# Kernel tuning notes

Hardware: AMD Instinct MI355X
Metric: run time of the kernel (lower is better)

Reference implementation:

```python
import jax, jax.numpy as jnp
import numpy as np

MU_P = 0.15
MASK_ID = 103
VOCAB = 30522


def setup_inputs() -> dict:
    key = jax.random.key(0)
    k1, k2 = jax.random.split(key)
    B, C, S = 1024, 4, 2048
    # first half = per-token sampling weights, second half = shared_tokens (unused by the math)
    my_attention_mask = jax.random.uniform(k1, (B, C, 2 * S), dtype=jnp.float32)
    attention_mask = jnp.ones((B, C, S), dtype=jnp.int32)  # tokenizer attention mask
    input_ids = jax.random.randint(k2, (B, C, S), 0, VOCAB, dtype=jnp.int32)
    return {"my_attention_mask": my_attention_mask,
            "attention_mask": attention_mask,
            "input_ids": input_ids}


def reference(my_attention_mask, attention_mask, input_ids):
    """Weighted sampling WITHOUT replacement per (batch, choice) row via Gumbel-top-k.

    Original loops over (k, j), draws num_to_mask = floor(sum(tok_mask) * N(mu_p, sigma))
    indices from the nonzero weights in my_attention_mask[..., :S] (prob ~ weight),
    masks those token positions in input_ids and emits the indicator mask.
    Gumbel-top-k: keys = log(w) + Gumbel noise; the top-num_to_mask keys are a
    weighted sample without replacement from w. Zero-weight positions get -inf keys.
    """
    B, C, S = input_ids.shape
    w = my_attention_mask[..., :S]  # [B, C, S] sampling weights

    key = jax.random.key(42)
    kg, kn = jax.random.split(key)
    sigma = min(0.05, MU_P / 4.0)
    frac = MU_P + sigma * jax.random.normal(kn, (B, C), dtype=jnp.float32)
    num_to_mask = jnp.floor(
        attention_mask.sum(axis=-1).astype(jnp.float32) * frac
    ).astype(jnp.int32)  # [B, C]

    log_w = jnp.where(w > 0, jnp.log(jnp.maximum(w, 1e-30)), -jnp.inf)
    keys = log_w + jax.random.gumbel(kg, w.shape, dtype=jnp.float32)  # [B, C, S]

    # rank[i] = position of i in descending key order (double argsort)
    order = jnp.argsort(-keys, axis=-1)
    rank = jnp.argsort(order, axis=-1)
    new_attention_mask = (rank < num_to_mask[..., None]).astype(jnp.int32)  # [B, C, S]

    new_input_ids = jnp.where(new_attention_mask == 1, MASK_ID, input_ids)
    discriminator_labels = -new_attention_mask
    return new_input_ids, new_attention_mask, discriminator_labels
```

## Files before the change

kernel.cpp:

```cpp
#include <hip/hip_runtime.h>
#include <stdint.h>
#include <math.h>

#define SLEN 2048
#define EPT 32
#define NTHREADS 256
#define ROWS_PER_BLOCK 4
#define NCHUNK 8
#define TOKENS_PER_OUT 8388608

__host__ __device__ __forceinline__ void tf2x32(uint32_t k0, uint32_t k1,
                                                uint32_t x0, uint32_t x1,
                                                uint32_t &o0, uint32_t &o1) {
  uint32_t ks2 = 0x1BD11BDAu ^ k0 ^ k1;
  x0 += k0; x1 += k1;
#define TFR(r) { x0 += x1; x1 = (x1 << (r)) | (x1 >> (32 - (r))); x1 ^= x0; }
  TFR(13) TFR(15) TFR(26) TFR(6)
  x0 += k1;  x1 += ks2 + 1u;
  TFR(17) TFR(29) TFR(16) TFR(24)
  x0 += ks2; x1 += k0 + 2u;
  TFR(13) TFR(15) TFR(26) TFR(6)
  x0 += k0;  x1 += k1 + 3u;
  TFR(17) TFR(29) TFR(16) TFR(24)
  x0 += k1;  x1 += ks2 + 4u;
  TFR(13) TFR(15) TFR(26) TFR(6)
  x0 += ks2; x1 += k0 + 5u;
#undef TFR
  o0 = x0; o1 = x1;
}

__device__ __forceinline__ void tf4_bits(uint32_t k0, uint32_t k1,
                                         uint32_t cbase, uint32_t bits[4]) {
  const uint32_t ks2 = 0x1BD11BDAu ^ k0 ^ k1;
  uint32_t x0[4], x1[4];
#pragma unroll
  for (int i = 0; i < 4; ++i) { x0[i] = k0; x1[i] = (cbase + (uint32_t)i) + k1; }
#define TFR4(r)                                                         \
  _Pragma("unroll")                                                     \
  for (int i = 0; i < 4; ++i) {                                         \
    x0[i] += x1[i];                                                     \
    x1[i] = (x1[i] << (r)) | (x1[i] >> (32 - (r)));                     \
    x1[i] ^= x0[i];                                                     \
  }                                                                     \
  __builtin_amdgcn_sched_barrier(0);
#define INJ4(a, b)                                                      \
  _Pragma("unroll")                                                     \
  for (int i = 0; i < 4; ++i) { x0[i] += (a); x1[i] += (b); }
  TFR4(13) TFR4(15) TFR4(26) TFR4(6)
  INJ4(k1, ks2 + 1u)
  TFR4(17) TFR4(29) TFR4(16) TFR4(24)
  INJ4(ks2, k0 + 2u)
  TFR4(13) TFR4(15) TFR4(26) TFR4(6)
  INJ4(k0, k1 + 3u)
  TFR4(17) TFR4(29) TFR4(16) TFR4(24)
  INJ4(k1, ks2 + 4u)
  TFR4(13) TFR4(15) TFR4(26) TFR4(6)
  INJ4(ks2, k0 + 5u)
#undef TFR4
#undef INJ4
#pragma unroll
  for (int i = 0; i < 4; ++i) bits[i] = x0[i] ^ x1[i];
}

__device__ __forceinline__ float u01_from_bits(uint32_t bits) {
  return __uint_as_float((bits >> 9) | 0x3F800000u) - 1.0f;
}

#define SBAR() __builtin_amdgcn_sched_barrier(0)

template<int CTRL, int RMASK>
__device__ __forceinline__ uint32_t dpp_mov0(uint32_t x) {
  return (uint32_t)__builtin_amdgcn_update_dpp(0, (int)x, CTRL, RMASK, 0xF, false);
}
__device__ __forceinline__ uint32_t wave_incl_scan(uint32_t x) {
  x += dpp_mov0<0x111, 0xF>(x);
  x += dpp_mov0<0x112, 0xF>(x);
  x += dpp_mov0<0x114, 0xF>(x);
  x += dpp_mov0<0x118, 0xF>(x);
  x += dpp_mov0<0x142, 0xA>(x);
  x += dpp_mov0<0x143, 0xC>(x);
  return x;
}

__device__ __forceinline__ void log8_cr(const float x[8], float out[8]) {
#pragma clang fp contract(off)
  double m[8]; int e[8];
#pragma unroll
  for (int i = 0; i < 8; ++i) {
    uint32_t xb   = __float_as_uint(x[i]);
    uint32_t mant = xb & 0x7FFFFFu;
    int      ee   = (int)(xb >> 23) - 127;
    bool     big  = mant > 0x3504F3u;
    e[i] = ee + (big ? 1 : 0);
    uint32_t hi = (big ? 0x3FE00000u : 0x3FF00000u) | (mant >> 3);
    uint32_t lo = mant << 29;
    m[i] = __longlong_as_double(((long long)hi << 32) | (long long)lo);
  }
  SBAR();
  double mp1[8];
#pragma unroll
  for (int i = 0; i < 8; ++i) mp1[i] = m[i] + 1.0;
  SBAR();
  double y[8];
#pragma unroll
  for (int i = 0; i < 8; ++i) y[i] = __builtin_amdgcn_rcp(mp1[i]);
  SBAR();
#pragma unroll
  for (int i = 0; i < 8; ++i) y[i] = fma(fma(-mp1[i], y[i], 1.0), y[i], y[i]);
  SBAR();
  double r[8];
#pragma unroll
  for (int i = 0; i < 8; ++i) r[i] = (m[i] - 1.0) * y[i];
  SBAR();
  double t[8];
#pragma unroll
  for (int i = 0; i < 8; ++i) t[i] = r[i] * r[i];
  SBAR();
  double p[8];
#pragma unroll
  for (int i = 0; i < 8; ++i) p[i] = fma(0.07692307692307693, t[i], 0.09090909090909091);
  SBAR();
#pragma unroll
  for (int i = 0; i < 8; ++i) p[i] = fma(p[i], t[i], 0.1111111111111111);
  SBAR();
#pragma unroll
  for (int i = 0; i < 8; ++i) p[i] = fma(p[i], t[i], 0.14285714285714285);
  SBAR();
#pragma unroll
  for (int i = 0; i < 8; ++i) p[i] = fma(p[i], t[i], 0.2);
  SBAR();
#pragma unroll
  for (int i = 0; i < 8; ++i) p[i] = fma(p[i], t[i], 0.3333333333333333);
  SBAR();
#pragma unroll
  for (int i = 0; i < 8; ++i) p[i] = fma(p[i], t[i], 1.0);
  SBAR();
#pragma unroll
  for (int i = 0; i < 8; ++i) r[i] = r[i] + r[i];
  SBAR();
#pragma unroll
  for (int i = 0; i < 8; ++i) p[i] = r[i] * p[i];
  SBAR();
#pragma unroll
  for (int i = 0; i < 8; ++i)
    out[i] = (float)fma((double)e[i], 0.6931471805599453, p[i]);
}

__device__ __forceinline__ float log_cr(float x) {
#pragma clang fp contract(off)
  uint32_t xb   = __float_as_uint(x);
  uint32_t mant = xb & 0x7FFFFFu;
  int      e    = (int)(xb >> 23) - 127;
  bool     big  = mant > 0x3504F3u;
  e += big ? 1 : 0;
  uint32_t hi = (big ? 0x3FE00000u : 0x3FF00000u) | (mant >> 3);
  double m = __longlong_as_double(((long long)hi << 32) | (long long)(mant << 29));
  double mp1 = m + 1.0;
  double y = __builtin_amdgcn_rcp(mp1);
  y = fma(fma(-mp1, y, 1.0), y, y);
  double r = (m - 1.0) * y;
  double t = r * r;
  double p = fma(0.07692307692307693, t, 0.09090909090909091);
  p = fma(p, t, 0.1111111111111111);
  p = fma(p, t, 0.14285714285714285);
  p = fma(p, t, 0.2);
  p = fma(p, t, 0.3333333333333333);
  p = fma(p, t, 1.0);
  return (float)fma((double)e, 0.6931471805599453, (r + r) * p);
}

__device__ float erfinv_xla(float x) {
#pragma clang fp contract(off)
  float x2  = x * x;
  float nx2 = -x2;
  float l1p;
  if (fabsf(nx2) < 1e-4f) {
    l1p = (-0.5f * nx2 + 1.0f) * nx2;
  } else {
    l1p = log_cr(1.0f + nx2);
  }
  float w = -l1p;
  float p;
  if (w < 5.0f) {
    float ww = w - 2.5f;
    p = 2.81022636e-08f;
    p = p * ww + 3.43273939e-07f;
    p = p * ww + -3.5233877e-06f;
    p = p * ww + -4.39150654e-06f;
    p = p * ww + 0.00021858087f;
    p = p * ww + -0.00125372503f;
    p = p * ww + -0.00417768164f;
    p = p * ww + 0.246640727f;
    p = p * ww + 1.50140941f;
  } else {
    float ww = sqrtf(w) - 3.0f;
    p = -0.000200214257f;
    p = p * ww + 0.000100950558f;
    p = p * ww + 0.00134934322f;
    p = p * ww + -0.00367342844f;
    p = p * ww + 0.00573950773f;
    p = p * ww + -0.0076224613f;
    p = p * ww + 0.00943887047f;
    p = p * ww + 1.00167406f;
    p = p * ww + 2.83297682f;
  }
  return p * x;
}

__global__ __launch_bounds__(NTHREADS, 4)
void gumbel_topk_mask(const float* __restrict__ wfull,
                      const int*   __restrict__ attn,
                      const int*   __restrict__ ids,
                      int* __restrict__ out,
                      uint32_t kg0, uint32_t kg1, uint32_t kn0, uint32_t kn1) {
#pragma clang fp contract(off)
  const int t    = threadIdx.x;
  const int lane = t & 63;
  const int wid  = t >> 6;
  const int row  = blockIdx.x * ROWS_PER_BLOCK + wid;

  __shared__ __align__(16) uint32_t hist[ROWS_PER_BLOCK][4][256];

  const size_t rbase = (size_t)row * SLEN;
  const size_t wbase = (size_t)row * (2 * SLEN);

#pragma unroll
  for (int p4 = 0; p4 < 4; ++p4)
    ((uint4*)hist[wid][p4])[lane] = make_uint4(0u, 0u, 0u, 0u);

  const int4*   av4 = (const int4*)(attn + rbase);
  const float4* wv4 = (const float4*)(wfull + wbase);
  const int4*   iv4 = (const int4*)(ids + rbase);

  int psum = 0;
#pragma unroll
  for (int j = 0; j < NCHUNK; ++j) {
    int4 a = av4[64 * j + lane];
    psum += a.x + a.y + a.z + a.w;
  }
  float4 wC[NCHUNK];
#pragma unroll
  for (int j = 0; j < NCHUNK; ++j) wC[j] = wv4[64 * j + lane];

  uint32_t no0, no1;
  tf2x32(kn0, kn1, 0u, (uint32_t)row, no0, no1);
  float f0  = u01_from_bits(no0 ^ no1);
  float lo  = __uint_as_float(0xBF7FFFFFu);
  float u2  = fmaxf(lo, f0 * 2.0f + lo);
  float z   = erfinv_xla(u2);
  float nrm = 1.4142135623730951f * z;
  float frac = 0.15f + 0.0375f * nrm;

  uint32_t ps = wave_incl_scan((uint32_t)psum);
  int asum = (int)__builtin_amdgcn_readlane((int)ps, 63);
  int kk = (int)floorf((float)asum * frac);

  uint32_t mloc[EPT];
#pragma unroll
  for (int c = 0; c < 4; ++c) {
    float4 wa = wC[2 * c], wb = wC[2 * c + 1];
    uint32_t bits[8];
    tf4_bits(kg0, kg1, (uint32_t)(rbase + 256 * (2 * c)     + 4 * lane), bits + 0);
    tf4_bits(kg0, kg1, (uint32_t)(rbase + 256 * (2 * c + 1) + 4 * lane), bits + 4);
    SBAR();
    float wl8[8] = {wa.x, wa.y, wa.z, wa.w, wb.x, wb.y, wb.z, wb.w};
    float uu[8];
#pragma unroll
    for (int e = 0; e < 8; ++e) {
      float f = u01_from_bits(bits[e]);
      uu[e] = fmaxf(1.17549435e-38f, f * 1.0f + 1.17549435e-38f);
    }
    SBAR();
    float l1[8];
    log8_cr(uu, l1);
    float wm[8];
#pragma unroll
    for (int e = 0; e < 8; ++e) wm[e] = fmaxf(wl8[e], 1e-30f);
    float lw[8];
    log8_cr(wm, lw);
    float nl1[8];
#pragma unroll
    for (int e = 0; e < 8; ++e) nl1[e] = -l1[e];
    float l2[8];
    log8_cr(nl1, l2);
    SBAR();
#pragma unroll
    for (int e = 0; e < 8; ++e) {
      float key = (wl8[e] > 0.0f) ? (lw[e] + (-l2[e])) : -__builtin_inff();
      uint32_t kb = __float_as_uint(key);
      mloc[8 * c + e] = (kb & 0x80000000u) ? ~kb : (kb | 0x80000000u);
    }
  }

  int4 idsv[NCHUNK];
#pragma unroll
  for (int j = 0; j < NCHUNK; ++j) idsv[j] = iv4[64 * j + lane];

  uint32_t T, r;
  if (kk <= 0)          { T = 0xFFFFFFFFu; r = 0u; }
  else if (kk >= SLEN)  { T = 0u;          r = (uint32_t)SLEN; }
  else {
    T = 0u;
    uint32_t need = (uint32_t)kk;
    asm volatile("s_waitcnt lgkmcnt(0)" ::: "memory");
#pragma unroll
    for (int e = 0; e < EPT; ++e)
      atomicAdd(&hist[wid][3][mloc[e] >> 24], 1u);
    for (int p = 3; ; --p) {
      asm volatile("s_waitcnt lgkmcnt(0)" ::: "memory");
      __builtin_amdgcn_wave_barrier();
      SBAR();
      uint4 hq = ((const uint4*)hist[wid][p])[lane];
      uint32_t gs = hq.x + hq.y + hq.z + hq.w;
      uint32_t P     = wave_incl_scan(gs);
      uint32_t total = (uint32_t)__builtin_amdgcn_readlane((int)P, 63);
      uint32_t Gex   = total - P;
      uint32_t S3 = Gex;
      uint32_t S2 = S3 + hq.w;
      uint32_t S1 = S2 + hq.z;
      uint32_t S0 = S1 + hq.y;
      uint32_t hh[4] = {hq.x, hq.y, hq.z, hq.w};
      uint32_t SS[4] = {S0, S1, S2, S3};
      int haswin = 0; uint32_t binv = 0u, remv = 0u; int donev = 0;
#pragma unroll
      for (int i = 0; i < 4; ++i) {
        if (hh[i] && SS[i] < need && need <= SS[i] + hh[i]) {
          haswin = 1;
          binv = (uint32_t)(4 * lane + i);
          remv = need - SS[i];
          donev = (remv == hh[i]) ? 1 : 0;
        }
      }
      unsigned long long wmask = __ballot(haswin);
      int src = (int)(__ffsll((unsigned long long)wmask) - 1);
      uint32_t bin = (uint32_t)__builtin_amdgcn_readlane((int)binv, src);
      uint32_t rem = (uint32_t)__builtin_amdgcn_readlane((int)remv, src);
      int     done = __builtin_amdgcn_readlane(donev, src);
      T |= bin << (8 * p);
      need = rem;
      if (done || p == 0) { r = rem; break; }
      const int sh = 8 * p;
#pragma unroll
      for (int e = 0; e < EPT; ++e) {
        uint32_t m = mloc[e];
        if ((m >> sh) == (T >> sh))
          atomicAdd(&hist[wid][p - 1][(m >> (sh - 8)) & 255u], 1u);
      }
    }
  }

  uint32_t cnt[NCHUNK];
#pragma unroll
  for (int j = 0; j < NCHUNK; ++j) {
    uint32_t c = 0;
#pragma unroll
    for (int e = 0; e < 4; ++e) c += (mloc[4 * j + e] == T) ? 1u : 0u;
    cnt[j] = c;
  }
  uint32_t incl[4];
#pragma unroll
  for (int q = 0; q < 4; ++q)
    incl[q] = wave_incl_scan(cnt[2 * q] | (cnt[2 * q + 1] << 16));
  uint32_t Spre[NCHUNK], tot[NCHUNK];
#pragma unroll
  for (int q = 0; q < 4; ++q) {
    uint32_t t63 = (uint32_t)__builtin_amdgcn_readlane((int)incl[q], 63);
    tot[2 * q]      = t63 & 0xFFFFu;
    tot[2 * q + 1]  = t63 >> 16;
    Spre[2 * q]     = (incl[q] & 0xFFFFu) - cnt[2 * q];
    Spre[2 * q + 1] = (incl[q] >> 16)     - cnt[2 * q + 1];
  }

  int4* po = (int4*)(out + rbase);
  int4* pm = (int4*)(out + TOKENS_PER_OUT + rbase);
  int4* pl = (int4*)(out + 2 * TOKENS_PER_OUT + rbase);
  uint32_t C = 0;
#pragma unroll
  for (int j = 0; j < NCHUNK; ++j) {
    uint32_t excl = C + Spre[j];
    int4 iv = idsv[j];
    int idv[4] = {iv.x, iv.y, iv.z, iv.w};
    int oid[4], omk[4], olb[4];
#pragma unroll
    for (int e = 0; e < 4; ++e) {
      uint32_t m = mloc[4 * j + e];
      bool eq  = (m == T);
      bool msk = (m > T) || (eq && (excl < r));
      excl += eq ? 1u : 0u;
      oid[e] = msk ? 103 : idv[e];
      omk[e] = msk ? 1 : 0;
      olb[e] = msk ? -1 : 0;
    }
    po[64 * j + lane] = make_int4(oid[0], oid[1], oid[2], oid[3]);
    pm[64 * j + lane] = make_int4(omk[0], omk[1], omk[2], omk[3]);
    pl[64 * j + lane] = make_int4(olb[0], olb[1], olb[2], olb[3]);
    C += tot[j];
  }
}

extern "C" void kernel_launch(void* const* d_in, const int* in_sizes, int n_in,
                              void* d_out, int out_size, void* d_ws, size_t ws_size,
                              hipStream_t stream) {
  (void)n_in; (void)d_ws; (void)ws_size; (void)out_size;
  const float* wfull = (const float*)d_in[0];
  const int*   attn  = (const int*)d_in[1];
  const int*   ids   = (const int*)d_in[2];
  int* out = (int*)d_out;

  uint32_t kg0, kg1, kn0, kn1, o0, o1;
  tf2x32(0u, 42u, 0u, 0u, o0, o1); kg0 = o0; kg1 = o1;
  tf2x32(0u, 42u, 0u, 1u, o0, o1); kn0 = o0; kn1 = o1;

  int rows = in_sizes[1] / SLEN;
  hipLaunchKernelGGL(gumbel_topk_mask, dim3(rows / ROWS_PER_BLOCK), dim3(NTHREADS),
                     0, stream, wfull, attn, ids, out, kg0, kg1, kn0, kn1);
}
```

Baseline: 200.3 us.

## Replace LDS radix-histogram select with bit-transposed bitwise radix select

Replaces the 4-pass 8-bit LDS histogram radix select (atomics into shared memory, wave barriers, scans) with a register-only approach. The 32 keys per lane are bit-transposed into 32 bitplanes, and a 32-step MSB-first bitwise select finds the k-th threshold using popcount plus a wave scan per bit. This removes the LDS atomics and the shared histogram. In exchange it always runs 32 wave scans and a 160-op transpose, where the old loop could stop early at coarser digits.

```diff
diff --git a/kernel.cpp b/kernel.cpp
--- a/kernel.cpp
+++ b/kernel.cpp
@@ -219,14 +219,8 @@
   const int wid  = t >> 6;
   const int row  = blockIdx.x * ROWS_PER_BLOCK + wid;
 
-  __shared__ __align__(16) uint32_t hist[ROWS_PER_BLOCK][4][256];
-
   const size_t rbase = (size_t)row * SLEN;
   const size_t wbase = (size_t)row * (2 * SLEN);
-
-#pragma unroll
-  for (int p4 = 0; p4 < 4; ++p4)
-    ((uint4*)hist[wid][p4])[lane] = make_uint4(0u, 0u, 0u, 0u);
 
   const int4*   av4 = (const int4*)(attn + rbase);
   const float4* wv4 = (const float4*)(wfull + wbase);
@@ -296,67 +290,49 @@
 #pragma unroll
   for (int j = 0; j < NCHUNK; ++j) idsv[j] = iv4[64 * j + lane];
 
-  uint32_t T, r;
-  if (kk <= 0)          { T = 0xFFFFFFFFu; r = 0u; }
-  else if (kk >= SLEN)  { T = 0u;          r = (uint32_t)SLEN; }
-  else {
-    T = 0u;
-    uint32_t need = (uint32_t)kk;
-    asm volatile("s_waitcnt lgkmcnt(0)" ::: "memory");
-#pragma unroll
-    for (int e = 0; e < EPT; ++e)
-      atomicAdd(&hist[wid][3][mloc[e] >> 24], 1u);
-    for (int p = 3; ; --p) {
-      asm volatile("s_waitcnt lgkmcnt(0)" ::: "memory");
-      __builtin_amdgcn_wave_barrier();
-      SBAR();
-      uint4 hq = ((const uint4*)hist[wid][p])[lane];
-      uint32_t gs = hq.x + hq.y + hq.z + hq.w;
-      uint32_t P     = wave_incl_scan(gs);
-      uint32_t total = (uint32_t)__builtin_amdgcn_readlane((int)P, 63);
-      uint32_t Gex   = total - P;
-      uint32_t S3 = Gex;
-      uint32_t S2 = S3 + hq.w;
-      uint32_t S1 = S2 + hq.z;
-      uint32_t S0 = S1 + hq.y;
-      uint32_t hh[4] = {hq.x, hq.y, hq.z, hq.w};
-      uint32_t SS[4] = {S0, S1, S2, S3};
-      int haswin = 0; uint32_t binv = 0u, remv = 0u; int donev = 0;
-#pragma unroll
-      for (int i = 0; i < 4; ++i) {
-        if (hh[i] && SS[i] < need && need <= SS[i] + hh[i]) {
-          haswin = 1;
-          binv = (uint32_t)(4 * lane + i);
-          remv = need - SS[i];
-          donev = (remv == hh[i]) ? 1 : 0;
+  {
+    const uint32_t MSK[5] = {0x0000FFFFu, 0x00FF00FFu, 0x0F0F0F0Fu,
+                             0x33333333u, 0x55555555u};
+#pragma unroll
+    for (int jj = 0; jj < 5; ++jj) {
+      const int j = 16 >> jj;
+      const uint32_t m = MSK[jj];
+#pragma unroll
+      for (int k = 0; k < 32; ++k) {
+        if ((k & j) == 0) {
+          uint32_t tt = (mloc[k] ^ (mloc[k + j] >> j)) & m;
+          mloc[k]     ^= tt;
+          mloc[k + j] ^= (tt << j);
         }
       }
-      unsigned long long wmask = __ballot(haswin);
-      int src = (int)(__ffsll((unsigned long long)wmask) - 1);
-      uint32_t bin = (uint32_t)__builtin_amdgcn_readlane((int)binv, src);
-      uint32_t rem = (uint32_t)__builtin_amdgcn_readlane((int)remv, src);
-      int     done = __builtin_amdgcn_readlane(donev, src);
-      T |= bin << (8 * p);
-      need = rem;
-      if (done || p == 0) { r = rem; break; }
-      const int sh = 8 * p;
-#pragma unroll
-      for (int e = 0; e < EPT; ++e) {
-        uint32_t m = mloc[e];
-        if ((m >> sh) == (T >> sh))
-          atomicAdd(&hist[wid][p - 1][(m >> (sh - 8)) & 255u], 1u);
-      }
-    }
+    }
+  }
+
+  uint32_t above, active, r;
+  if (kk <= 0)          { above = 0u;          active = 0u; r = 0u; }
+  else if (kk >= SLEN)  { above = 0xFFFFFFFFu; active = 0u; r = 0u; }
+  else {
+    above = 0u; active = 0xFFFFFFFFu;
+    uint32_t need = (uint32_t)kk;
+#pragma unroll
+    for (int b = 31; b >= 0; --b) {
+      uint32_t M    = mloc[31 - b];
+      uint32_t cand = active & M;
+      uint32_t c    = (uint32_t)__popc(cand);
+      uint32_t P    = wave_incl_scan(c);
+      uint32_t tot  = (uint32_t)__builtin_amdgcn_readlane((int)P, 63);
+      bool hi = (need <= tot);
+      above  = hi ? above : (above | cand);
+      need   = hi ? need  : (need - tot);
+      active = hi ? cand  : (active & ~M);
+    }
+    r = need;
   }
 
   uint32_t cnt[NCHUNK];
 #pragma unroll
-  for (int j = 0; j < NCHUNK; ++j) {
-    uint32_t c = 0;
-#pragma unroll
-    for (int e = 0; e < 4; ++e) c += (mloc[4 * j + e] == T) ? 1u : 0u;
-    cnt[j] = c;
-  }
+  for (int j = 0; j < NCHUNK; ++j)
+    cnt[j] = (uint32_t)__popc(active & (0xFu << (28 - 4 * j)));
   uint32_t incl[4];
 #pragma unroll
   for (int q = 0; q < 4; ++q)
@@ -383,9 +359,10 @@
     int oid[4], omk[4], olb[4];
 #pragma unroll
     for (int e = 0; e < 4; ++e) {
-      uint32_t m = mloc[4 * j + e];
-      bool eq  = (m == T);
-      bool msk = (m > T) || (eq && (excl < r));
+      const int bit = 31 - (4 * j + e);
+      bool eq  = (active >> bit) & 1u;
+      bool abv = (above  >> bit) & 1u;
+      bool msk = abv || (eq && (excl < r));
       excl += eq ? 1u : 0u;
       oid[e] = msk ? 103 : idv[e];
       omk[e] = msk ? 1 : 0;
```

Result: slower. 214.8 us (+7.2%).
